# Kernel tuning notes

Measured on AMD Instinct MI355X. Metric: run time of the kernel, lower is better.

Reference implementation:

```python
import jax, jax.numpy as jnp
import numpy as np

B, S, H = 2, 2048, 2048
NH, NKV, HD = 16, 4, 128
EPS = 1e-6


def setup_inputs() -> dict:
    key = jax.random.key(0)
    ks = jax.random.split(key, 8)
    s = 0.02
    x = jax.random.normal(ks[0], (B, S, H), dtype=jnp.float32)
    # real rotary tables: cos/sin of shape [S, HD]
    inv_freq = 1.0 / (10000.0 ** (np.arange(0, HD, 2, dtype=np.float32) / HD))
    t = np.arange(S, dtype=np.float32)
    freqs = np.outer(t, inv_freq)              # [S, HD/2]
    emb = np.concatenate([freqs, freqs], axis=-1)  # [S, HD]
    rotary_cos = jnp.asarray(np.cos(emb))
    rotary_sin = jnp.asarray(np.sin(emb))
    Wq = jax.random.normal(ks[1], (H, NH * HD), dtype=jnp.float32) * s
    Wk = jax.random.normal(ks[2], (H, NKV * HD), dtype=jnp.float32) * s
    Wv = jax.random.normal(ks[3], (H, NKV * HD), dtype=jnp.float32) * s
    Wo = jax.random.normal(ks[4], (H, H), dtype=jnp.float32) * s
    q_norm_w = jnp.ones((HD,), dtype=jnp.float32)
    k_norm_w = jnp.ones((HD,), dtype=jnp.float32)
    return {"x": x, "rotary_cos": rotary_cos, "rotary_sin": rotary_sin,
            "Wq": Wq, "Wk": Wk, "Wv": Wv, "Wo": Wo,
            "q_norm_w": q_norm_w, "k_norm_w": k_norm_w}


def _rms_norm(x, w):
    return x * jax.lax.rsqrt(jnp.mean(x * x, axis=-1, keepdims=True) + EPS) * w


def _rotate_half(x):
    half = x.shape[-1] // 2
    return jnp.concatenate([-x[..., half:], x[..., :half]], axis=-1)


def reference(x, rotary_cos, rotary_sin, Wq, Wk, Wv, Wo, q_norm_w, k_norm_w):
    b, s, _ = x.shape
    q = (x @ Wq).reshape(b, s, NH, HD)
    k = (x @ Wk).reshape(b, s, NKV, HD)
    v = (x @ Wv).reshape(b, s, NKV, HD)
    q = _rms_norm(q, q_norm_w)
    k = _rms_norm(k, k_norm_w)
    cos = rotary_cos[None, :, None, :]  # [1,S,1,HD]
    sin = rotary_sin[None, :, None, :]
    q = q * cos + _rotate_half(q) * sin
    k = k * cos + _rotate_half(k) * sin
    # GQA: repeat kv heads
    rep = NH // NKV
    k = jnp.repeat(k, rep, axis=2)  # [b,s,NH,HD]
    v = jnp.repeat(v, rep, axis=2)
    scores = jnp.einsum('bqhd,bkhd->bhqk', q, k) / jnp.sqrt(jnp.float32(HD))
    causal = jnp.tril(jnp.ones((s, s), dtype=bool))
    scores = jnp.where(causal[None, None], scores, -jnp.inf)
    probs = jax.nn.softmax(scores.astype(jnp.float32), axis=-1).astype(q.dtype)
    y = jnp.einsum('bhqk,bkhd->bqhd', probs, v).reshape(b, s, NH * HD)
    return y @ Wo
```

## Files before the change

kernel.cpp:

```cpp
#include <hip/hip_runtime.h>


#define S_LEN 2048

typedef __bf16 bf16_t;
typedef bf16_t bf16x8 __attribute__((ext_vector_type(8)));
typedef float f32x4 __attribute__((ext_vector_type(4)));
typedef float f32x16 __attribute__((ext_vector_type(16)));
typedef unsigned int u32x4 __attribute__((ext_vector_type(4)));
typedef unsigned short u16x4 __attribute__((ext_vector_type(4)));

__device__ __forceinline__ unsigned short f2bf(float f) {
  unsigned int u = __builtin_bit_cast(unsigned int, f);
  u += 0x7fffu + ((u >> 16) & 1u);
  return (unsigned short)(u >> 16);
}
__device__ __forceinline__ float bf2f(unsigned short h) {
  return __builtin_bit_cast(float, (unsigned int)h << 16);
}
__device__ __forceinline__ unsigned pk2(float a, float b) {
  return (unsigned)f2bf(a) | ((unsigned)f2bf(b) << 16);
}
__device__ __forceinline__ unsigned cvtpk(float a, float b) {
  unsigned r;
  asm("v_cvt_pk_bf16_f32 %0, %1, %2" : "=v"(r) : "v"(a), "v"(b));
  return r;
}

typedef const __attribute__((address_space(1))) unsigned int* gas1_t;
typedef __attribute__((address_space(3))) unsigned int* las3_t;
__device__ __forceinline__ void async16(const void* g, void* l) {
  __builtin_amdgcn_global_load_lds((gas1_t)g, (las3_t)l, 16, 0, 0);
}

__device__ __forceinline__ bf16x8 ldfrag(const void* p) {
  return __builtin_bit_cast(bf16x8, *(const u32x4*)p);
}
__device__ __forceinline__ f32x16 mfma32(bf16x8 a, bf16x8 b, f32x16 c) {
  return __builtin_amdgcn_mfma_f32_32x32x16_bf16(a, b, c, 0, 0, 0);
}
__device__ __forceinline__ f32x16 zero16() {
  f32x16 v;
#pragma unroll
  for (int i = 0; i < 16; i++) v[i] = 0.f;
  return v;
}

__global__ __launch_bounds__(256) void cast_x_kernel(
    const float* __restrict__ in, unsigned short* __restrict__ out, int n8) {
  int i = blockIdx.x * 256 + threadIdx.x;
  if (i >= n8) return;
  const f32x4* p = (const f32x4*)in + (size_t)i * 2;
  f32x4 a = p[0], b = p[1];
  u32x4 o;
  o.x = pk2(a.x, a.y);
  o.y = pk2(a.z, a.w);
  o.z = pk2(b.x, b.y);
  o.w = pk2(b.z, b.w);
  *(u32x4*)(out + (size_t)i * 8) = o;
}

__global__ __launch_bounds__(256) void transpose_cast_kernel(
    const float* __restrict__ in, unsigned short* __restrict__ out,
    int R, int C, int out_row_off, int out_ld) {
  __shared__ unsigned short L[64][68];
  int t = threadIdx.x;
  int r0 = blockIdx.y * 64, c0 = blockIdx.x * 64;
#pragma unroll
  for (int i = 0; i < 4; i++) {
    int r = i * 16 + (t >> 4);
    int c = (t & 15) * 4;
    f32x4 v = *(const f32x4*)&in[(size_t)(r0 + r) * C + c0 + c];
    u16x4 u;
    u.x = f2bf(v.x); u.y = f2bf(v.y); u.z = f2bf(v.z); u.w = f2bf(v.w);
    *(u16x4*)&L[r][c] = u;
  }
  __syncthreads();
#pragma unroll
  for (int i = 0; i < 4; i++) {
    int oc = i * 16 + (t >> 4);
    int orr = (t & 15) * 4;
    u16x4 u;
    u.x = L[orr + 0][oc]; u.y = L[orr + 1][oc];
    u.z = L[orr + 2][oc]; u.w = L[orr + 3][oc];
    *(u16x4*)&out[(size_t)(c0 + oc + out_row_off) * out_ld + r0 + orr] = u;
  }
}

__global__ __launch_bounds__(256) void gemm_bf16_kernel(
    const unsigned short* __restrict__ A, const unsigned short* __restrict__ Bt,
    void* __restrict__ Cout, int M, int N, int K, int out_bf16) {
  __shared__ unsigned short As[2][128 * 32];
  __shared__ unsigned short Bs[2][128 * 32];
  const int t = threadIdx.x, w = t >> 6, l = t & 63;
  const int wr = w >> 1, wc = w & 1;
  const int lrow = l & 15, lhi = l >> 4;
  const int row0 = blockIdx.y * 128, col0 = blockIdx.x * 128;
  const unsigned short* Ab = A + (size_t)row0 * K;
  const unsigned short* Bb = Bt + (size_t)col0 * K;
  const int srow = w * 32 + (l >> 2);
  const int scol = (l & 3) * 8;
  f32x4 z = {0.f, 0.f, 0.f, 0.f};
  f32x4 acc[4][4];
#pragma unroll
  for (int m = 0; m < 4; m++)
#pragma unroll
    for (int n = 0; n < 4; n++) acc[m][n] = z;

#define STAGE_G(tt, buf)                                                        \
  {                                                                             \
    const int k0_ = (tt) * 32;                                                  \
    async16(Ab + (size_t)srow * K + k0_ + scol,        &As[buf][(w * 32) * 32]);\
    async16(Ab + (size_t)(srow + 16) * K + k0_ + scol, &As[buf][(w * 32 + 16) * 32]); \
    async16(Bb + (size_t)srow * K + k0_ + scol,        &Bs[buf][(w * 32) * 32]);\
    async16(Bb + (size_t)(srow + 16) * K + k0_ + scol, &Bs[buf][(w * 32 + 16) * 32]); \
  }

  STAGE_G(0, 0);
  const int NT = K >> 5;
  for (int tt = 0; tt < NT; tt++) {
    const int cur = tt & 1;
    if (tt + 1 < NT) {
      STAGE_G(tt + 1, cur ^ 1);
      asm volatile("s_waitcnt vmcnt(4)" ::: "memory");
    } else {
      asm volatile("s_waitcnt vmcnt(0)" ::: "memory");
    }
    __builtin_amdgcn_s_barrier();
    __builtin_amdgcn_sched_barrier(0);
    bf16x8 af[4], bfr[4];
#pragma unroll
    for (int m = 0; m < 4; m++)
      af[m] = ldfrag(&As[cur][(wr * 64 + m * 16 + lrow) * 32 + lhi * 8]);
#pragma unroll
    for (int n = 0; n < 4; n++)
      bfr[n] = ldfrag(&Bs[cur][(wc * 64 + n * 16 + lrow) * 32 + lhi * 8]);
    __builtin_amdgcn_s_setprio(1);
#pragma unroll
    for (int m = 0; m < 4; m++)
#pragma unroll
      for (int n = 0; n < 4; n++)
        acc[m][n] = __builtin_amdgcn_mfma_f32_16x16x32_bf16(af[m], bfr[n], acc[m][n], 0, 0, 0);
    __builtin_amdgcn_s_setprio(0);
    __builtin_amdgcn_sched_barrier(0);
    __builtin_amdgcn_s_barrier();
  }
#undef STAGE_G

  if (out_bf16) {
    unsigned short* C = (unsigned short*)Cout;
#pragma unroll
    for (int m = 0; m < 4; m++)
#pragma unroll
      for (int n = 0; n < 4; n++)
#pragma unroll
        for (int r = 0; r < 4; r++) {
          size_t grow = row0 + wr * 64 + m * 16 + lhi * 4 + r;
          size_t gcol = col0 + wc * 64 + n * 16 + lrow;
          C[grow * N + gcol] = f2bf(acc[m][n][r]);
        }
  } else {
    float* C = (float*)Cout;
#pragma unroll
    for (int m = 0; m < 4; m++)
#pragma unroll
      for (int n = 0; n < 4; n++)
#pragma unroll
        for (int r = 0; r < 4; r++) {
          size_t grow = row0 + wr * 64 + m * 16 + lhi * 4 + r;
          size_t gcol = col0 + wc * 64 + n * 16 + lrow;
          C[grow * N + gcol] = acc[m][n][r];
        }
  }
}

__global__ __launch_bounds__(256) void mid_kernel(
    const unsigned short* __restrict__ QKV, const float* __restrict__ cosT,
    const float* __restrict__ sinT, const float* __restrict__ qw,
    const float* __restrict__ kw, unsigned short* __restrict__ Qpk,
    unsigned short* __restrict__ Kpk, unsigned short* __restrict__ Vpk) {
  int w = threadIdx.x >> 6, l = threadIdx.x & 63;
  int g = blockIdx.x * 4 + w;
  int bs = g / 24, idx = g - bs * 24;
  int b = bs >> 11, s = bs & 2047;
  int d0 = 2 * l;
  unsigned int uu = *(const unsigned int*)(QKV + (size_t)bs * 3072 + idx * 128 + d0);
  float x0 = bf2f((unsigned short)(uu & 0xffffu));
  float x1 = bf2f((unsigned short)(uu >> 16));
  if (idx < 20) {
    const float* nw = (idx < 16) ? qw : kw;
    float ss = x0 * x0 + x1 * x1;
#pragma unroll
    for (int mk = 1; mk < 64; mk <<= 1) ss += __shfl_xor(ss, mk);
    float inv = rsqrtf(ss * (1.0f / 128.0f) + 1e-6f);
    float n0 = x0 * inv * nw[d0], n1 = x1 * inv * nw[d0 + 1];
    float p0 = __shfl_xor(n0, 32), p1 = __shfl_xor(n1, 32);
    float sg = (l < 32) ? -1.0f : 1.0f;
    float c0 = cosT[s * 128 + d0], c1 = cosT[s * 128 + d0 + 1];
    float sn0 = sinT[s * 128 + d0], sn1 = sinT[s * 128 + d0 + 1];
    float o0 = n0 * c0 + sg * p0 * sn0;
    float o1 = n1 * c1 + sg * p1 * sn1;
    int mf = d0 >> 4, hi = (d0 >> 3) & 1, j = d0 & 7;
    int blk = s >> 5, r31 = s & 31;
    int foff = (mf * 2 + hi) * 256 + r31 * 8 + j;
    unsigned short* dst;
    if (idx < 16) {
      const float qs = 0.08838834764831845f * 1.4426950408889634f;
      o0 *= qs; o1 *= qs;
      dst = Qpk + (((size_t)(b * 16 + idx)) * 64 + blk) * 4096 + foff;
    } else {
      dst = Kpk + (((size_t)(b * 4 + (idx - 16))) * 64 + blk) * 4096 + foff;
    }
    *(unsigned int*)dst = pk2(o0, o1);
  } else {
    int kvh = idx - 20;
    int blk = s >> 5, ks = (s >> 4) & 1, his = (s >> 3) & 1, j = s & 7;
    int n = d0 >> 5, d31 = d0 & 31;
    size_t base = (((size_t)(b * 4 + kvh)) * 64 + blk) * 4096 +
                  (((n * 2 + ks) * 2 + his) * 256 + d31 * 8 + j);
    Vpk[base] = f2bf(x0);
    Vpk[base + 8] = f2bf(x1);
  }
}

__global__ __launch_bounds__(512) void attn_kernel(
    const unsigned short* __restrict__ Qpk, const unsigned short* __restrict__ Kpk,
    const unsigned short* __restrict__ Vpk, unsigned short* __restrict__ Y) {
  __shared__ __attribute__((aligned(16))) unsigned char lds_raw[100352];
  const int t = threadIdx.x, w = t >> 6, l = t & 63;
  const int q31 = l & 31, hi = l >> 5;
  const int grp = w >> 2, hw = w & 3;
  const int bid = blockIdx.x;
  const int xcd = bid & 7;
  const int b = xcd >> 2, kvh = xcd & 3;
  const int hd = kvh * 4 + hw;
  const int bh = b * 16 + hd;
  const int pj = bid >> 3;
  const unsigned short* Kg = Kpk + (size_t)(b * 4 + kvh) * 262144;
  const unsigned short* Vg = Vpk + (size_t)(b * 4 + kvh) * 262144;
  float* mlb = (float*)(lds_raw + 98304);

#define STAGE1(st, buf)                                                        \
  {                                                                            \
    unsigned char* base_ = lds_raw + ((buf) * 2 + grp) * 16384;                \
    const unsigned short* kg_ = Kg + (size_t)(st) * 4096;                      \
    const unsigned short* vg_ = Vg + (size_t)(st) * 4096;                      \
    _Pragma("unroll")                                                          \
    for (int i_ = 0; i_ < 4; i_++) {                                           \
      int c_ = hw * 4 + i_;                                                    \
      const unsigned short* src_ = (c_ < 8) ? (kg_ + c_ * 512 + l * 8)         \
                                            : (vg_ + (c_ - 8) * 512 + l * 8);  \
      async16(src_, base_ + c_ * 1024 + l * 16);                               \
    }                                                                          \
  }

  for (int phase = 0; phase < 2; phase++) {
    const int strip = phase ? pj : (63 - pj);
    const int q0w = strip * 32;
    const int qg = q0w + q31;
    const int nt = strip + 1;
    const int hcut = (nt + 1) >> 1;
    const int myFirst = grp ? hcut : 0;
    const int myCnt = grp ? (nt - hcut) : hcut;
    const int R = hcut;

    const unsigned short* Qs = Qpk + (((size_t)bh * 64 + strip) * 4096) + (size_t)l * 8;
    bf16x8 qf[8];
#pragma unroll
    for (int mf = 0; mf < 8; mf++) qf[mf] = ldfrag(Qs + mf * 512);
    asm volatile("s_waitcnt vmcnt(0)" ::: "memory");

    { int st0 = (myCnt > 0) ? myFirst : 0; STAGE1(st0, 0); }

    f32x16 o[4];
#pragma unroll
    for (int n = 0; n < 4; n++) o[n] = zero16();
    float m = -3.0e38f, lsum = 0.f;

    for (int r = 0; r < R; r++) {
      const int buf = r % 3;
      { int st = (r + 1 < myCnt) ? (myFirst + r + 1) : 0; STAGE1(st, (r + 1) % 3); }
      asm volatile("s_waitcnt vmcnt(4)" ::: "memory");
      __builtin_amdgcn_s_barrier();
      __builtin_amdgcn_sched_barrier(0);

      if (r < myCnt) {
        const int ti = myFirst + r;
        const int kv0 = ti << 5;
        const unsigned short* base =
            (const unsigned short*)(lds_raw + (buf * 2 + grp) * 16384);
        f32x16 sA = zero16(), sB = zero16();
        __builtin_amdgcn_s_setprio(1);
#pragma unroll
        for (int mf = 0; mf < 4; mf++) {
          sA = mfma32(ldfrag(base + mf * 512 + l * 8), qf[mf], sA);
          sB = mfma32(ldfrag(base + (mf + 4) * 512 + l * 8), qf[mf + 4], sB);
        }
        __builtin_amdgcn_s_setprio(0);
#pragma unroll
        for (int rr = 0; rr < 16; rr++) sA[rr] += sB[rr];
        if (ti == nt - 1) {
#pragma unroll
          for (int rr = 0; rr < 16; rr++) {
            int kv = kv0 + (rr & 3) + 8 * (rr >> 2) + 4 * hi;
            if (kv > qg) sA[rr] = -3.0e38f;
          }
        }
        float pm = sA[0];
#pragma unroll
        for (int rr = 1; rr < 16; rr++) pm = fmaxf(pm, sA[rr]);
        pm = fmaxf(pm, __shfl_xor(pm, 32));
        if (__any(pm > m + 8.0f)) {
          float mn = fmaxf(m, pm);
          float scl = exp2f(m - mn);
          m = mn; lsum *= scl;
#pragma unroll
          for (int rr = 0; rr < 16; rr++) {
            float sr = __shfl(scl, (rr & 3) + 8 * (rr >> 2) + 4 * hi);
            o[0][rr] *= sr; o[1][rr] *= sr; o[2][rr] *= sr; o[3][rr] *= sr;
          }
        }
#pragma unroll
        for (int rr = 0; rr < 16; rr++) sA[rr] = exp2f(sA[rr] - m);
        float ts = 0.f;
#pragma unroll
        for (int rr = 0; rr < 16; rr++) ts += sA[rr];
        ts += __shfl_xor(ts, 32);
        lsum += ts;
        bf16x8 paf[2];
#pragma unroll
        for (int f = 0; f < 2; f++) {
          const int bs8 = 8 * f;
          unsigned g00 = cvtpk(sA[bs8 + 0], sA[bs8 + 1]);
          unsigned g01 = cvtpk(sA[bs8 + 2], sA[bs8 + 3]);
          unsigned g10 = cvtpk(sA[bs8 + 4], sA[bs8 + 5]);
          unsigned g11 = cvtpk(sA[bs8 + 6], sA[bs8 + 7]);
          unsigned snd0 = hi ? g00 : g10;
          unsigned snd1 = hi ? g01 : g11;
          unsigned r0 = (unsigned)__shfl_xor((int)snd0, 32);
          unsigned r1 = (unsigned)__shfl_xor((int)snd1, 32);
          unsigned own0 = hi ? g10 : g00;
          unsigned own1 = hi ? g11 : g01;
          u32x4 wv;
          wv.x = hi ? r0 : own0;
          wv.y = hi ? r1 : own1;
          wv.z = hi ? own0 : r0;
          wv.w = hi ? own1 : r1;
          paf[f] = __builtin_bit_cast(bf16x8, wv);
        }
        __builtin_amdgcn_s_setprio(1);
#pragma unroll
        for (int n = 0; n < 4; n++) {
          o[n] = mfma32(paf[0], ldfrag(base + 4096 + (n * 2 + 0) * 512 + l * 8), o[n]);
          o[n] = mfma32(paf[1], ldfrag(base + 4096 + (n * 2 + 1) * 512 + l * 8), o[n]);
        }
        __builtin_amdgcn_s_setprio(0);
      }
    }

    __syncthreads();
    if (l < 32) {
      mlb[hw * 128 + grp * 64 + q31] = m;
      mlb[hw * 128 + grp * 64 + 32 + q31] = lsum;
    }
    __syncthreads();
    float m_o = mlb[hw * 128 + (grp ^ 1) * 64 + q31];
    float l_o = mlb[hw * 128 + (grp ^ 1) * 64 + 32 + q31];
    float M = fmaxf(m, m_o);
    float sc = exp2f(m - M);
    float lF = lsum * sc + l_o * exp2f(m_o - M);
#pragma unroll
    for (int rr = 0; rr < 16; rr++) {
      float sr = __shfl(sc, (rr & 3) + 8 * (rr >> 2) + 4 * hi);
      o[0][rr] *= sr; o[1][rr] *= sr; o[2][rr] *= sr; o[3][rr] *= sr;
    }
    float* ob = (float*)lds_raw + hw * 4096;
    if (grp == 1) {
#pragma unroll
      for (int rr = 0; rr < 16; rr++) {
        int cr = (rr & 3) + 8 * (rr >> 2) + 4 * hi;
#pragma unroll
        for (int n = 0; n < 4; n++) ob[cr * 128 + n * 32 + q31] = o[n][rr];
      }
    }
    __syncthreads();
    if (grp == 0) {
      float linv = 1.0f / lF;
#pragma unroll
      for (int rr = 0; rr < 16; rr++) {
        int cr = (rr & 3) + 8 * (rr >> 2) + 4 * hi;
        float lr = __shfl(linv, cr);
        int qrow = q0w + cr;
        size_t rowoff = ((size_t)(b * S_LEN + qrow)) * 2048 + hd * 128 + q31;
        Y[rowoff]      = f2bf((o[0][rr] + ob[cr * 128 + q31]) * lr);
        Y[rowoff + 32] = f2bf((o[1][rr] + ob[cr * 128 + 32 + q31]) * lr);
        Y[rowoff + 64] = f2bf((o[2][rr] + ob[cr * 128 + 64 + q31]) * lr);
        Y[rowoff + 96] = f2bf((o[3][rr] + ob[cr * 128 + 96 + q31]) * lr);
      }
    }
    __syncthreads();
  }
#undef STAGE1
}

extern "C" void kernel_launch(void* const* d_in, const int* in_sizes, int n_in,
                              void* d_out, int out_size, void* d_ws, size_t ws_size,
                              hipStream_t stream) {
  const float* x  = (const float*)d_in[0];
  const float* rc = (const float*)d_in[1];
  const float* rs = (const float*)d_in[2];
  const float* Wq = (const float*)d_in[3];
  const float* Wk = (const float*)d_in[4];
  const float* Wv = (const float*)d_in[5];
  const float* Wo = (const float*)d_in[6];
  const float* qw = (const float*)d_in[7];
  const float* kw = (const float*)d_in[8];
  float* out = (float*)d_out;
  char* ws = (char*)d_ws;

  unsigned short* xb   = (unsigned short*)(ws + 0);
  unsigned short* WT   = (unsigned short*)(ws + 16777216);
  unsigned short* WoT  = (unsigned short*)(ws + 29360128);
  unsigned short* QKVb = (unsigned short*)(ws + 37748736);
  unsigned short* Qpk  = (unsigned short*)(ws + 0);
  unsigned short* Kpk  = (unsigned short*)(ws + 16777216);
  unsigned short* Vpk  = (unsigned short*)(ws + 20971520);
  unsigned short* Yb   = (unsigned short*)(ws + 37748736);

  cast_x_kernel<<<4096, 256, 0, stream>>>(x, xb, 1048576);
  transpose_cast_kernel<<<dim3(32, 32), 256, 0, stream>>>(Wq, WT, 2048, 2048, 0, 2048);
  transpose_cast_kernel<<<dim3(8, 32), 256, 0, stream>>>(Wk, WT, 2048, 512, 2048, 2048);
  transpose_cast_kernel<<<dim3(8, 32), 256, 0, stream>>>(Wv, WT, 2048, 512, 2560, 2048);
  transpose_cast_kernel<<<dim3(32, 32), 256, 0, stream>>>(Wo, WoT, 2048, 2048, 0, 2048);
  gemm_bf16_kernel<<<dim3(24, 32), 256, 0, stream>>>(xb, WT, QKVb, 4096, 3072, 2048, 1);
  mid_kernel<<<24576, 256, 0, stream>>>(QKVb, rc, rs, qw, kw, Qpk, Kpk, Vpk);
  attn_kernel<<<256, 512, 0, stream>>>(Qpk, Kpk, Vpk, Yb);
  gemm_bf16_kernel<<<dim3(16, 32), 256, 0, stream>>>(Yb, WoT, out, 4096, 2048, 2048, 0);
}
```

Baseline: 224.9 us.

## Split attention KV range across three wave groups and merge prep kernels

The attention kernel grows from 8 to 12 waves per block and divides each strip's KV tiles among three groups instead of two. The LDS stage buffers, the max/sum exchange and the output reduction are extended to merge three partial softmax results. Separately, the x cast and the four weight transpose-cast kernels are folded into a single prep launch to cut launch overhead. The larger LDS footprint (about 147 KB) and 768-thread blocks may cap occupancy and per-wave registers, and the three-way merge adds epilogue work.

```diff
diff --git a/kernel.cpp b/kernel.cpp
--- a/kernel.cpp
+++ b/kernel.cpp
@@ -46,26 +46,11 @@
   return v;
 }
 
-__global__ __launch_bounds__(256) void cast_x_kernel(
-    const float* __restrict__ in, unsigned short* __restrict__ out, int n8) {
-  int i = blockIdx.x * 256 + threadIdx.x;
-  if (i >= n8) return;
-  const f32x4* p = (const f32x4*)in + (size_t)i * 2;
-  f32x4 a = p[0], b = p[1];
-  u32x4 o;
-  o.x = pk2(a.x, a.y);
-  o.y = pk2(a.z, a.w);
-  o.z = pk2(b.x, b.y);
-  o.w = pk2(b.z, b.w);
-  *(u32x4*)(out + (size_t)i * 8) = o;
-}
-
-__global__ __launch_bounds__(256) void transpose_cast_kernel(
+__device__ __forceinline__ void transpose_body(
     const float* __restrict__ in, unsigned short* __restrict__ out,
-    int R, int C, int out_row_off, int out_ld) {
-  __shared__ unsigned short L[64][68];
-  int t = threadIdx.x;
-  int r0 = blockIdx.y * 64, c0 = blockIdx.x * 64;
+    int C, int out_row_off, int out_ld, int bx, int by, int t,
+    unsigned short (*L)[68]) {
+  int r0 = by * 64, c0 = bx * 64;
 #pragma unroll
   for (int i = 0; i < 4; i++) {
     int r = i * 16 + (t >> 4);
@@ -84,6 +69,38 @@
     u.x = L[orr + 0][oc]; u.y = L[orr + 1][oc];
     u.z = L[orr + 2][oc]; u.w = L[orr + 3][oc];
     *(u16x4*)&out[(size_t)(c0 + oc + out_row_off) * out_ld + r0 + orr] = u;
+  }
+}
+
+__global__ __launch_bounds__(256) void prep_kernel(
+    const float* __restrict__ x, const float* __restrict__ Wq,
+    const float* __restrict__ Wk, const float* __restrict__ Wv,
+    const float* __restrict__ Wo, unsigned short* __restrict__ xb,
+    unsigned short* __restrict__ WT, unsigned short* __restrict__ WoT) {
+  __shared__ unsigned short L[64][68];
+  const int bid = blockIdx.x, t = threadIdx.x;
+  if (bid < 4096) {
+    int i = bid * 256 + t;
+    const f32x4* p = (const f32x4*)x + (size_t)i * 2;
+    f32x4 a = p[0], b = p[1];
+    u32x4 o;
+    o.x = pk2(a.x, a.y);
+    o.y = pk2(a.z, a.w);
+    o.z = pk2(b.x, b.y);
+    o.w = pk2(b.z, b.w);
+    *(u32x4*)(xb + (size_t)i * 8) = o;
+  } else if (bid < 5120) {
+    int id = bid - 4096;
+    transpose_body(Wq, WT, 2048, 0, 2048, id & 31, id >> 5, t, L);
+  } else if (bid < 5376) {
+    int id = bid - 5120;
+    transpose_body(Wk, WT, 512, 2048, 2048, id & 7, id >> 3, t, L);
+  } else if (bid < 5632) {
+    int id = bid - 5376;
+    transpose_body(Wv, WT, 512, 2560, 2048, id & 7, id >> 3, t, L);
+  } else {
+    int id = bid - 5632;
+    transpose_body(Wo, WoT, 2048, 0, 2048, id & 31, id >> 5, t, L);
   }
 }
 
@@ -223,10 +240,10 @@
   }
 }
 
-__global__ __launch_bounds__(512) void attn_kernel(
+__global__ __launch_bounds__(768) void attn_kernel(
     const unsigned short* __restrict__ Qpk, const unsigned short* __restrict__ Kpk,
     const unsigned short* __restrict__ Vpk, unsigned short* __restrict__ Y) {
-  __shared__ __attribute__((aligned(16))) unsigned char lds_raw[100352];
+  __shared__ __attribute__((aligned(16))) unsigned char lds_raw[150528];
   const int t = threadIdx.x, w = t >> 6, l = t & 63;
   const int q31 = l & 31, hi = l >> 5;
   const int grp = w >> 2, hw = w & 3;
@@ -238,11 +255,11 @@
   const int pj = bid >> 3;
   const unsigned short* Kg = Kpk + (size_t)(b * 4 + kvh) * 262144;
   const unsigned short* Vg = Vpk + (size_t)(b * 4 + kvh) * 262144;
-  float* mlb = (float*)(lds_raw + 98304);
+  float* mlb = (float*)(lds_raw + 147456);
 
 #define STAGE1(st, buf)                                                        \
   {                                                                            \
-    unsigned char* base_ = lds_raw + ((buf) * 2 + grp) * 16384;                \
+    unsigned char* base_ = lds_raw + ((buf) * 3 + grp) * 16384;                \
     const unsigned short* kg_ = Kg + (size_t)(st) * 4096;                      \
     const unsigned short* vg_ = Vg + (size_t)(st) * 4096;                      \
     _Pragma("unroll")                                                          \
@@ -259,10 +276,14 @@
     const int q0w = strip * 32;
     const int qg = q0w + q31;
     const int nt = strip + 1;
-    const int hcut = (nt + 1) >> 1;
-    const int myFirst = grp ? hcut : 0;
-    const int myCnt = grp ? (nt - hcut) : hcut;
-    const int R = hcut;
+    const int base3 = nt / 3, rem = nt - 3 * base3;
+    const int cnt0 = base3 + (rem > 0 ? 1 : 0);
+    const int cnt1 = base3 + (rem > 1 ? 1 : 0);
+    int myFirst, myCnt;
+    if (grp == 0)      { myFirst = 0;           myCnt = cnt0; }
+    else if (grp == 1) { myFirst = cnt0;        myCnt = cnt1; }
+    else               { myFirst = cnt0 + cnt1; myCnt = base3; }
+    const int R = cnt0;
 
     const unsigned short* Qs = Qpk + (((size_t)bh * 64 + strip) * 4096) + (size_t)l * 8;
     bf16x8 qf[8];
@@ -288,7 +309,7 @@
         const int ti = myFirst + r;
         const int kv0 = ti << 5;
         const unsigned short* base =
-            (const unsigned short*)(lds_raw + (buf * 2 + grp) * 16384);
+            (const unsigned short*)(lds_raw + (buf * 3 + grp) * 16384);
         f32x16 sA = zero16(), sB = zero16();
         __builtin_amdgcn_s_setprio(1);
 #pragma unroll
@@ -360,22 +381,23 @@
 
     __syncthreads();
     if (l < 32) {
-      mlb[hw * 128 + grp * 64 + q31] = m;
-      mlb[hw * 128 + grp * 64 + 32 + q31] = lsum;
+      mlb[(hw * 3 + grp) * 64 + q31] = m;
+      mlb[(hw * 3 + grp) * 64 + 32 + q31] = lsum;
     }
     __syncthreads();
-    float m_o = mlb[hw * 128 + (grp ^ 1) * 64 + q31];
-    float l_o = mlb[hw * 128 + (grp ^ 1) * 64 + 32 + q31];
-    float M = fmaxf(m, m_o);
+    float m0 = mlb[(hw * 3 + 0) * 64 + q31], l0 = mlb[(hw * 3 + 0) * 64 + 32 + q31];
+    float m1 = mlb[(hw * 3 + 1) * 64 + q31], l1 = mlb[(hw * 3 + 1) * 64 + 32 + q31];
+    float m2 = mlb[(hw * 3 + 2) * 64 + q31], l2 = mlb[(hw * 3 + 2) * 64 + 32 + q31];
+    float M = fmaxf(m0, fmaxf(m1, m2));
     float sc = exp2f(m - M);
-    float lF = lsum * sc + l_o * exp2f(m_o - M);
+    float lF = l0 * exp2f(m0 - M) + l1 * exp2f(m1 - M) + l2 * exp2f(m2 - M);
 #pragma unroll
     for (int rr = 0; rr < 16; rr++) {
       float sr = __shfl(sc, (rr & 3) + 8 * (rr >> 2) + 4 * hi);
       o[0][rr] *= sr; o[1][rr] *= sr; o[2][rr] *= sr; o[3][rr] *= sr;
     }
-    float* ob = (float*)lds_raw + hw * 4096;
-    if (grp == 1) {
+    if (grp > 0) {
+      float* ob = (float*)(lds_raw + ((grp - 1) * 4 + hw) * 16384);
 #pragma unroll
       for (int rr = 0; rr < 16; rr++) {
         int cr = (rr & 3) + 8 * (rr >> 2) + 4 * hi;
@@ -385,6 +407,8 @@
     }
     __syncthreads();
     if (grp == 0) {
+      const float* ob1 = (const float*)(lds_raw + (0 * 4 + hw) * 16384);
+      const float* ob2 = (const float*)(lds_raw + (1 * 4 + hw) * 16384);
       float linv = 1.0f / lF;
 #pragma unroll
       for (int rr = 0; rr < 16; rr++) {
@@ -392,10 +416,10 @@
         float lr = __shfl(linv, cr);
         int qrow = q0w + cr;
         size_t rowoff = ((size_t)(b * S_LEN + qrow)) * 2048 + hd * 128 + q31;
-        Y[rowoff]      = f2bf((o[0][rr] + ob[cr * 128 + q31]) * lr);
-        Y[rowoff + 32] = f2bf((o[1][rr] + ob[cr * 128 + 32 + q31]) * lr);
-        Y[rowoff + 64] = f2bf((o[2][rr] + ob[cr * 128 + 64 + q31]) * lr);
-        Y[rowoff + 96] = f2bf((o[3][rr] + ob[cr * 128 + 96 + q31]) * lr);
+        Y[rowoff]      = f2bf((o[0][rr] + ob1[cr * 128 + q31]      + ob2[cr * 128 + q31]) * lr);
+        Y[rowoff + 32] = f2bf((o[1][rr] + ob1[cr * 128 + 32 + q31] + ob2[cr * 128 + 32 + q31]) * lr);
+        Y[rowoff + 64] = f2bf((o[2][rr] + ob1[cr * 128 + 64 + q31] + ob2[cr * 128 + 64 + q31]) * lr);
+        Y[rowoff + 96] = f2bf((o[3][rr] + ob1[cr * 128 + 96 + q31] + ob2[cr * 128 + 96 + q31]) * lr);
       }
     }
     __syncthreads();
@@ -427,13 +451,9 @@
   unsigned short* Vpk  = (unsigned short*)(ws + 20971520);
   unsigned short* Yb   = (unsigned short*)(ws + 37748736);
 
-  cast_x_kernel<<<4096, 256, 0, stream>>>(x, xb, 1048576);
-  transpose_cast_kernel<<<dim3(32, 32), 256, 0, stream>>>(Wq, WT, 2048, 2048, 0, 2048);
-  transpose_cast_kernel<<<dim3(8, 32), 256, 0, stream>>>(Wk, WT, 2048, 512, 2048, 2048);
-  transpose_cast_kernel<<<dim3(8, 32), 256, 0, stream>>>(Wv, WT, 2048, 512, 2560, 2048);
-  transpose_cast_kernel<<<dim3(32, 32), 256, 0, stream>>>(Wo, WoT, 2048, 2048, 0, 2048);
+  prep_kernel<<<6656, 256, 0, stream>>>(x, Wq, Wk, Wv, Wo, xb, WT, WoT);
   gemm_bf16_kernel<<<dim3(24, 32), 256, 0, stream>>>(xb, WT, QKVb, 4096, 3072, 2048, 1);
   mid_kernel<<<24576, 256, 0, stream>>>(QKVb, rc, rs, qw, kw, Qpk, Kpk, Vpk);
-  attn_kernel<<<256, 512, 0, stream>>>(Qpk, Kpk, Vpk, Yb);
+  attn_kernel<<<256, 768, 0, stream>>>(Qpk, Kpk, Vpk, Yb);
   gemm_bf16_kernel<<<dim3(16, 32), 256, 0, stream>>>(Yb, WoT, out, 4096, 2048, 2048, 0);
 }
```

New measurement: 231.6 us. 3.0% more time.
